# Performance work log

Measured on AMD Instinct MI355X. Metric: run time of the kernel, lower is better.

The kernel has to match this reference:

```python
import jax, jax.numpy as jnp
import numpy as np

N, E, IN, OUT, R, B = 20000, 640000, 128, 128, 65, 65
BN_EPS = 1e-5


def setup_inputs() -> dict:
    key = jax.random.key(0)
    ks = jax.random.split(key, 8)
    node_feats = jax.random.normal(ks[0], (N, IN), dtype=jnp.float32)
    src = jax.random.randint(ks[1], (E,), 0, N, dtype=jnp.int32)
    dst = jax.random.randint(ks[2], (E,), 0, N, dtype=jnp.int32)
    etype = jax.random.randint(ks[3], (E,), 0, R, dtype=jnp.int32)
    norm = jax.random.uniform(ks[4], (E, 1), dtype=jnp.float32)
    basis = jax.random.normal(ks[5], (B, IN, OUT), dtype=jnp.float32) * 0.05
    comp = jax.random.normal(ks[6], (R, B), dtype=jnp.float32) * 0.1
    h_bias = jnp.zeros((OUT,), dtype=jnp.float32)
    W_res = jax.random.normal(ks[7], (IN, OUT), dtype=jnp.float32) * 0.05
    b_res = jnp.zeros((OUT,), dtype=jnp.float32)
    gamma = jnp.ones((OUT,), dtype=jnp.float32)
    beta = jnp.zeros((OUT,), dtype=jnp.float32)
    return dict(node_feats=node_feats, src=src, dst=dst, etype=etype, norm=norm,
                basis=basis, comp=comp, h_bias=h_bias, W_res=W_res, b_res=b_res,
                gamma=gamma, beta=beta)


def reference(node_feats, src, dst, etype, norm, basis, comp, h_bias, W_res, b_res, gamma, beta):
    n, in_f = node_feats.shape
    r = comp.shape[0]
    # Basis decomposition: W_r = sum_b comp[r,b] * basis[b]  -> (R, in, out)
    W = jnp.einsum('rb,bio->rio', comp, basis)
    # Per-edge message x[src] * norm (norm is scalar per edge so it commutes
    # with the relation matmul). Aggregate per (dst, relation) first, then do
    # one dense relation-batched GEMM (mathematically identical to DGL's
    # per-edge transform + scatter-add, since everything is linear).
    msg = node_feats[src] * norm                       # (E, in)
    seg = dst.astype(jnp.int32) * r + etype            # combined (dst, rel) key
    S = jax.ops.segment_sum(msg, seg, num_segments=n * r).reshape(n, r, in_f)
    h = jnp.einsum('nri,rio->no', S, W) + h_bias       # (N, out)
    h = jax.nn.relu(h)                                 # conv activation (dropout p=0)
    # Residual branch: relu(Linear(x))
    h = h + jax.nn.relu(node_feats @ W_res + b_res)
    # BatchNorm1d (training mode: batch stats, biased variance)
    mean = jnp.mean(h, axis=0)
    var = jnp.var(h, axis=0)
    h = (h - mean) * jax.lax.rsqrt(var + BN_EPS) * gamma + beta
    return h
```

## Files before the change

### kernel.cpp

```cpp
#include <hip/hip_runtime.h>
#include <hip/hip_bf16.h>


#define N_NODES 20000
#define E_EDGES 640000
#define R_REL   65
#define TM      64
#define NB_RESID 313
#define MAX_TILES 10240
#define SCAT_CH 2560

typedef __attribute__((ext_vector_type(8))) short bf16x8;
typedef __attribute__((ext_vector_type(4))) float f32x4;
typedef __attribute__((ext_vector_type(4))) unsigned int u32x4;
typedef __attribute__((ext_vector_type(2))) unsigned int u32x2;

__device__ __forceinline__ unsigned short f2bf(float x) {
    union { float f; unsigned int u; } c; c.f = x;
    unsigned int b = c.u + 0x7fffu + ((c.u >> 16) & 1u);
    return (unsigned short)(b >> 16);
}
__device__ __forceinline__ float bf2f_lo(unsigned int u) {
    union { unsigned int u; float f; } c; c.u = u << 16; return c.f;
}
__device__ __forceinline__ float bf2f_hi(unsigned int u) {
    union { unsigned int u; float f; } c; c.u = u & 0xffff0000u; return c.f;
}
__device__ __forceinline__ void async16(const void* g, void* l) {
    __builtin_amdgcn_global_load_lds(
        (const __attribute__((address_space(1))) unsigned int*)g,
        (__attribute__((address_space(3))) unsigned int*)l, 16, 0, 0);
}
__device__ __forceinline__ int unperm(int p) {
    return (p & 64) + ((p & 3) << 4) + ((p >> 2) & 15);
}

__global__ void k_prep1(const float* __restrict__ comp, const float* __restrict__ basis,
                        float* __restrict__ W32, const int* __restrict__ et,
                        const int* __restrict__ dstA, int* __restrict__ ghist,
                        int* __restrict__ gh2, const float* __restrict__ node_feats,
                        unsigned short* __restrict__ node_bf) {
    __shared__ float lc[16 * 65];
    __shared__ int lh[R_REL];
    int b = blockIdx.x, t = threadIdx.x;
    if (b < 320) {
        int r0 = (b >> 6) * 16;
        int col = (b & 63) * 256 + t;
        for (int j = t; j < 16 * 65; j += 256) {
            int rr = r0 + j / 65;
            lc[j] = (rr < R_REL) ? comp[rr * 65 + (j % 65)] : 0.f;
        }
        __syncthreads();
        float acc[16];
#pragma unroll
        for (int j = 0; j < 16; ++j) acc[j] = 0.f;
        for (int k = 0; k < 65; ++k) {
            float v = basis[k * 16384 + col];
#pragma unroll
            for (int j = 0; j < 16; ++j) acc[j] += lc[j * 65 + k] * v;
        }
#pragma unroll
        for (int j = 0; j < 16; ++j) {
            int rr = r0 + j;
            if (rr < R_REL) W32[rr * 16384 + col] = acc[j];
        }
    } else if (b < 832) {
        if (t < R_REL) lh[t] = 0;
        __syncthreads();
        for (int i = (b - 320) * 256 + t; i < E_EDGES; i += 512 * 256) {
            atomicAdd(&lh[et[i]], 1);
            atomicAdd(&gh2[dstA[i]], 1);
        }
        __syncthreads();
        if (t < R_REL) atomicAdd(&ghist[t], lh[t]);
    } else {
        int i = (b - 832) * 256 + t;
        if (i < N_NODES * 32) {
            float4 v = reinterpret_cast<const float4*>(node_feats)[i];
            __hip_bfloat162 b0 = __float22bfloat162_rn(make_float2(v.x, v.y));
            __hip_bfloat162 b1 = __float22bfloat162_rn(make_float2(v.z, v.w));
            u32x2 pk;
            pk.x = *reinterpret_cast<unsigned int*>(&b0);
            pk.y = *reinterpret_cast<unsigned int*>(&b1);
            reinterpret_cast<u32x2*>(node_bf)[i] = pk;
        }
    }
}

__global__ void k_prep3(const int* __restrict__ gh2, int* __restrict__ cnt2,
                        int* __restrict__ seg, const int* __restrict__ ghist,
                        int* __restrict__ cnt, int* __restrict__ ntiles_p,
                        int* __restrict__ tile_rel, int* __restrict__ tile_start,
                        int* __restrict__ tile_len, const float* __restrict__ W32,
                        unsigned short* __restrict__ Wt, const float* __restrict__ Wresf,
                        unsigned short* __restrict__ Wrest) {
    int b = blockIdx.x, t = threadIdx.x;
    if (b < 80) {
        __shared__ int red[256];
        __shared__ int pref;
        int acc = 0;
        for (int i = t; i < b * 256; i += 256) acc += gh2[i];
        red[t] = acc;
        __syncthreads();
        for (int off = 128; off > 0; off >>= 1) {
            if (t < off) red[t] += red[t + off];
            __syncthreads();
        }
        if (t == 0) pref = red[0];
        __syncthreads();
        int i = b * 256 + t;
        int v = (i < N_NODES) ? gh2[i] : 0;
        red[t] = v;
        __syncthreads();
        for (int off = 1; off < 256; off <<= 1) {
            int x = (t >= off) ? red[t - off] : 0;
            __syncthreads();
            red[t] += x;
            __syncthreads();
        }
        int excl = red[t] - v + pref;
        if (i < N_NODES) {
            cnt2[i] = excl;
            seg[i] = excl;
            if (i == N_NODES - 1) seg[N_NODES] = excl + v;
        }
    } else if (b == 80) {
        __shared__ int base[R_REL + 1], tbase[R_REL + 1];
        int lane = t & 63;
        if (t < 64) {
            int v = ghist[lane];
            int x = v;
#pragma unroll
            for (int off = 1; off < 64; off <<= 1) {
                int y = __shfl_up(x, off);
                if (lane >= off) x += y;
            }
            base[lane] = x - v;
            if (lane == 63) {
                base[64] = x;
                base[65] = x + ghist[64];
            }
        }
        __syncthreads();
        if (t == 0) {
            int tb = 0;
            for (int r = 0; r < R_REL; ++r) {
                tbase[r] = tb;
                tb += (base[r + 1] - base[r] + TM - 1) / TM;
            }
            *ntiles_p = tb;
        }
        __syncthreads();
        if (t < R_REL) {
            cnt[t] = base[t];
            int s = base[t], e = base[t + 1], j = tbase[t];
            while (s < e) {
                int len = min(TM, e - s);
                tile_rel[j] = t; tile_start[j] = s; tile_len[j] = len;
                ++j; s += len;
            }
        }
    } else {
        __shared__ float tile[64][65];
        int bb = b - 81;
        const float* s; unsigned short* d; int sub;
        if (bb < R_REL * 4) { s = W32 + (size_t)(bb >> 2) * 16384; d = Wt + (size_t)(bb >> 2) * 16384; sub = bb & 3; }
        else { s = Wresf; d = Wrest; sub = bb - R_REL * 4; }
        int ot = (sub >> 1) & 1, itl = sub & 1;
        int tx = t & 63, ty = t >> 6;
        for (int it = 0; it < 16; ++it) {
            int i = ty + it * 4;
            tile[i][tx] = s[(itl * 64 + i) * 128 + ot * 64 + tx];
        }
        __syncthreads();
        for (int it = 0; it < 16; ++it) {
            int o = ty + it * 4;
            d[(ot * 64 + o) * 128 + itl * 64 + tx] = f2bf(tile[tx][o]);
        }
    }
}

__global__ void k_scatter2(const int* __restrict__ et, const int* __restrict__ srcA,
                           const int* __restrict__ dstA, const float* __restrict__ norm,
                           int* __restrict__ cnt, int* __restrict__ cnt2,
                           int* __restrict__ srcp, float* __restrict__ normp,
                           int* __restrict__ inv2) {
    __shared__ int lh[R_REL], lbase[R_REL];
    int c0 = blockIdx.x * SCAT_CH;
    int cend = min(c0 + SCAT_CH, E_EDGES);
    if (threadIdx.x < R_REL) lh[threadIdx.x] = 0;
    __syncthreads();
    for (int i = c0 + threadIdx.x; i < cend; i += 256) atomicAdd(&lh[et[i]], 1);
    __syncthreads();
    if (threadIdx.x < R_REL && lh[threadIdx.x] > 0)
        lbase[threadIdx.x] = atomicAdd(&cnt[threadIdx.x], lh[threadIdx.x]);
    __syncthreads();
    if (threadIdx.x < R_REL) lh[threadIdx.x] = 0;
    __syncthreads();
    for (int i = c0 + threadIdx.x; i < cend; i += 256) {
        int r = et[i];
        int p = lbase[r] + atomicAdd(&lh[r], 1);
        srcp[p] = srcA[i];
        normp[p] = norm[i];
        inv2[p] = atomicAdd(&cnt2[dstA[i]], 1);
    }
}

__global__ __launch_bounds__(256, 3) void k_conv_gemm(
    const int* __restrict__ tile_rel, const int* __restrict__ tile_start,
    const int* __restrict__ tile_len, const int* __restrict__ ntiles_p,
    const int* __restrict__ srcp, const float* __restrict__ normp,
    const unsigned short* __restrict__ node_bf,
    const unsigned short* __restrict__ Wt, const unsigned short* __restrict__ Wrest,
    const float* __restrict__ b_res, const int* __restrict__ inv2,
    unsigned short* __restrict__ t_out, float* __restrict__ resid) {
    __shared__ unsigned short Alds[64 * 128];
    __shared__ unsigned short Blds[128 * 128];
    __shared__ float snorm[64];
    __shared__ int sp2[64];
    int t = threadIdx.x;
    int w = t >> 6, lane = t & 63;
    int wr = (w >> 1) * 32, wc = (w & 1) * 64;
    int lrow = lane & 15, quad = lane >> 4;

    if (blockIdx.x < NB_RESID) {
        int row0 = blockIdx.x * 64;
        int nrows = min(64, N_NODES - row0);
#pragma unroll
        for (int it = 0; it < 8; ++it) {
            int j = t + 256 * it;
            int o = j >> 4, c = j & 15, cs = c ^ (o & 15);
            async16(Wrest + o * 128 + cs * 8, &Blds[o * 128 + c * 8]);
        }
#pragma unroll
        for (int it = 0; it < 4; ++it) {
            int j = t + 256 * it;
            int p = j >> 4, c = j & 15, cs = c ^ (p & 15);
            if (p < nrows)
                async16(node_bf + (size_t)(row0 + p) * 128 + cs * 8,
                        &Alds[p * 128 + c * 8]);
        }
        __syncthreads();
        f32x4 acc[2][4];
#pragma unroll
        for (int i = 0; i < 2; ++i)
#pragma unroll
            for (int j = 0; j < 4; ++j) acc[i][j] = (f32x4){0.f, 0.f, 0.f, 0.f};
#pragma unroll
        for (int ks = 0; ks < 4; ++ks) {
            int cs = (ks * 4 + quad) ^ lrow;
            bf16x8 af[2], bfr[4];
#pragma unroll
            for (int i = 0; i < 2; ++i)
                af[i] = *reinterpret_cast<const bf16x8*>(&Alds[(wr + i * 16 + lrow) * 128 + cs * 8]);
#pragma unroll
            for (int j = 0; j < 4; ++j)
                bfr[j] = *reinterpret_cast<const bf16x8*>(&Blds[(wc + j * 16 + lrow) * 128 + cs * 8]);
#pragma unroll
            for (int i = 0; i < 2; ++i)
#pragma unroll
                for (int j = 0; j < 4; ++j)
                    acc[i][j] = __builtin_amdgcn_mfma_f32_16x16x32_bf16(af[i], bfr[j], acc[i][j], 0, 0, 0);
        }
        float br0 = b_res[wc + lrow];
        float br1 = b_res[wc + 16 + lrow];
        float br2 = b_res[wc + 32 + lrow];
        float br3 = b_res[wc + 48 + lrow];
#pragma unroll
        for (int i = 0; i < 2; ++i) {
#pragma unroll
            for (int reg = 0; reg < 4; ++reg) {
                int grow = row0 + wr + i * 16 + quad * 4 + reg;
                if (grow < N_NODES) {
                    float4 v;
                    v.x = fmaxf(acc[i][0][reg] + br0, 0.f);
                    v.y = fmaxf(acc[i][1][reg] + br1, 0.f);
                    v.z = fmaxf(acc[i][2][reg] + br2, 0.f);
                    v.w = fmaxf(acc[i][3][reg] + br3, 0.f);
                    *reinterpret_cast<float4*>(resid + (size_t)grow * 128 + wc + lrow * 4) = v;
                }
            }
        }
        return;
    }

    int tid = blockIdx.x - NB_RESID;
    if (tid >= *ntiles_p) return;
    int r = tile_rel[tid], start = tile_start[tid], len = tile_len[tid];
    const unsigned short* Wr = Wt + (size_t)r * 16384;
#pragma unroll
    for (int it = 0; it < 8; ++it) {
        int j = t + 256 * it;
        int o = j >> 4, c = j & 15, cs = c ^ (o & 15);
        async16(Wr + o * 128 + cs * 8, &Blds[o * 128 + c * 8]);
    }
#pragma unroll
    for (int it = 0; it < 4; ++it) {
        int j = t + 256 * it;
        int p = j >> 4, c = j & 15, cs = c ^ (p & 15);
        if (p < len)
            async16(node_bf + (size_t)srcp[start + p] * 128 + cs * 8,
                    &Alds[p * 128 + c * 8]);
    }
    if (t < TM && t < len) {
        snorm[t] = normp[start + t];
        sp2[t] = inv2[start + t];
    }
    __syncthreads();

    f32x4 acc[2][4];
#pragma unroll
    for (int i = 0; i < 2; ++i)
#pragma unroll
        for (int j = 0; j < 4; ++j) acc[i][j] = (f32x4){0.f, 0.f, 0.f, 0.f};
#pragma unroll
    for (int ks = 0; ks < 4; ++ks) {
        int cs = (ks * 4 + quad) ^ lrow;
        bf16x8 af[2], bfr[4];
#pragma unroll
        for (int i = 0; i < 2; ++i)
            af[i] = *reinterpret_cast<const bf16x8*>(&Alds[(wr + i * 16 + lrow) * 128 + cs * 8]);
#pragma unroll
        for (int j = 0; j < 4; ++j)
            bfr[j] = *reinterpret_cast<const bf16x8*>(&Blds[(wc + j * 16 + lrow) * 128 + cs * 8]);
#pragma unroll
        for (int i = 0; i < 2; ++i)
#pragma unroll
            for (int j = 0; j < 4; ++j)
                acc[i][j] = __builtin_amdgcn_mfma_f32_16x16x32_bf16(af[i], bfr[j], acc[i][j], 0, 0, 0);
    }

#pragma unroll
    for (int i = 0; i < 2; ++i) {
        int m0 = wr + i * 16 + quad * 4;
#pragma unroll
        for (int reg = 0; reg < 4; ++reg) {
            int m = m0 + reg;
            if (m < len) {
                float nm = snorm[m];
                int p2 = sp2[m];
                float2 lo2 = make_float2(acc[i][0][reg] * nm, acc[i][1][reg] * nm);
                float2 hi2 = make_float2(acc[i][2][reg] * nm, acc[i][3][reg] * nm);
                __hip_bfloat162 blo = __float22bfloat162_rn(lo2);
                __hip_bfloat162 bhi = __float22bfloat162_rn(hi2);
                u32x2 st;
                st.x = *reinterpret_cast<unsigned int*>(&blo);
                st.y = *reinterpret_cast<unsigned int*>(&bhi);
                *reinterpret_cast<u32x2*>(t_out + (size_t)p2 * 128 + wc + lrow * 4) = st;
            }
        }
    }
}

__global__ __launch_bounds__(256) void k_reduce_fused(
    const unsigned short* __restrict__ t, const int* __restrict__ seg,
    const float* __restrict__ resid, const float* __restrict__ h_bias,
    float* __restrict__ h, float* __restrict__ colsum, float* __restrict__ colsumsq) {
    __shared__ float cs1[128], cs2[128], sbias[128];
    if (threadIdx.x < 128) {
        cs1[threadIdx.x] = 0.f; cs2[threadIdx.x] = 0.f;
        sbias[threadIdx.x] = h_bias[unperm(threadIdx.x)];
    }
    __syncthreads();
    int w = threadIdx.x >> 6, lane = threadIdx.x & 63;
    int g = lane >> 4, c = lane & 15;
    for (int k = 0; k < 4; ++k) {
        int d = blockIdx.x * 16 + k * 4 + w;
        int a = seg[d], b = seg[d + 1];
        float s[8];
#pragma unroll
        for (int kk = 0; kk < 8; ++kk) s[kk] = 0.f;
        int q = a + g;
        for (; q + 28 < b; q += 32) {
            u32x4 v0 = *reinterpret_cast<const u32x4*>(t + (size_t)q * 128 + c * 8);
            u32x4 v1 = *reinterpret_cast<const u32x4*>(t + (size_t)(q + 4) * 128 + c * 8);
            u32x4 v2 = *reinterpret_cast<const u32x4*>(t + (size_t)(q + 8) * 128 + c * 8);
            u32x4 v3 = *reinterpret_cast<const u32x4*>(t + (size_t)(q + 12) * 128 + c * 8);
            u32x4 v4 = *reinterpret_cast<const u32x4*>(t + (size_t)(q + 16) * 128 + c * 8);
            u32x4 v5 = *reinterpret_cast<const u32x4*>(t + (size_t)(q + 20) * 128 + c * 8);
            u32x4 v6 = *reinterpret_cast<const u32x4*>(t + (size_t)(q + 24) * 128 + c * 8);
            u32x4 v7 = *reinterpret_cast<const u32x4*>(t + (size_t)(q + 28) * 128 + c * 8);
#pragma unroll
            for (int kk = 0; kk < 4; ++kk) {
                s[2 * kk]     += bf2f_lo(v0[kk]) + bf2f_lo(v1[kk]) + bf2f_lo(v2[kk]) + bf2f_lo(v3[kk])
                               + bf2f_lo(v4[kk]) + bf2f_lo(v5[kk]) + bf2f_lo(v6[kk]) + bf2f_lo(v7[kk]);
                s[2 * kk + 1] += bf2f_hi(v0[kk]) + bf2f_hi(v1[kk]) + bf2f_hi(v2[kk]) + bf2f_hi(v3[kk])
                               + bf2f_hi(v4[kk]) + bf2f_hi(v5[kk]) + bf2f_hi(v6[kk]) + bf2f_hi(v7[kk]);
            }
        }
        for (; q < b; q += 4) {
            u32x4 v = *reinterpret_cast<const u32x4*>(t + (size_t)q * 128 + c * 8);
#pragma unroll
            for (int kk = 0; kk < 4; ++kk) {
                s[2 * kk]     += bf2f_lo(v[kk]);
                s[2 * kk + 1] += bf2f_hi(v[kk]);
            }
        }
#pragma unroll
        for (int kk = 0; kk < 8; ++kk) {
            s[kk] += __shfl_xor(s[kk], 16);
            s[kk] += __shfl_xor(s[kk], 32);
        }
        if (g == 0) {
            const float* rp = resid + (size_t)d * 128 + c * 8;
            float4 r0 = *reinterpret_cast<const float4*>(rp);
            float4 r1 = *reinterpret_cast<const float4*>(rp + 4);
            float rr[8] = {r0.x, r0.y, r0.z, r0.w, r1.x, r1.y, r1.z, r1.w};
            float v[8];
#pragma unroll
            for (int kk = 0; kk < 8; ++kk)
                v[kk] = fmaxf(s[kk] + sbias[c * 8 + kk], 0.f) + rr[kk];
            float* hp = h + (size_t)d * 128 + c * 8;
            *reinterpret_cast<float4*>(hp)     = make_float4(v[0], v[1], v[2], v[3]);
            *reinterpret_cast<float4*>(hp + 4) = make_float4(v[4], v[5], v[6], v[7]);
#pragma unroll
            for (int kk = 0; kk < 8; ++kk) {
                atomicAdd(&cs1[c * 8 + kk], v[kk]);
                atomicAdd(&cs2[c * 8 + kk], v[kk] * v[kk]);
            }
        }
    }
    __syncthreads();
    if (threadIdx.x < 128) {
        atomicAdd(&colsum[threadIdx.x], cs1[threadIdx.x]);
        atomicAdd(&colsumsq[threadIdx.x], cs2[threadIdx.x]);
    }
}

__global__ void k_bn(float* __restrict__ h, const float* __restrict__ colsum,
                     const float* __restrict__ colsumsq, const float* __restrict__ gamma,
                     const float* __restrict__ beta) {
    __shared__ float sc[128], sh[128], tile[8][128];
    int t = threadIdx.x;
    if (t < 128) {
        int n = unperm(t);
        float m = colsum[t] * (1.f / N_NODES);
        float var = colsumsq[t] * (1.f / N_NODES) - m * m;
        float s = gamma[n] * rsqrtf(var + 1e-5f);
        sc[t] = s;
        sh[t] = beta[n] - m * s;
    }
    __syncthreads();
    int r = t >> 5;
    int p0 = (t & 31) * 4;
    int n0 = (p0 & 64) + ((p0 >> 2) & 15);
    for (int row0 = blockIdx.x * 8; row0 < N_NODES; row0 += gridDim.x * 8) {
        int row = row0 + r;
        float4 v = make_float4(0.f, 0.f, 0.f, 0.f);
        if (row < N_NODES) v = *reinterpret_cast<float4*>(h + (size_t)row * 128 + p0);
        v.x = v.x * sc[p0] + sh[p0];
        v.y = v.y * sc[p0 + 1] + sh[p0 + 1];
        v.z = v.z * sc[p0 + 2] + sh[p0 + 2];
        v.w = v.w * sc[p0 + 3] + sh[p0 + 3];
        tile[r][n0]      = v.x;
        tile[r][n0 + 16] = v.y;
        tile[r][n0 + 32] = v.z;
        tile[r][n0 + 48] = v.w;
        __syncthreads();
        if (row < N_NODES)
            *reinterpret_cast<float4*>(h + (size_t)row * 128 + p0) =
                *reinterpret_cast<float4*>(&tile[r][p0]);
        __syncthreads();
    }
}

extern "C" void kernel_launch(void* const* d_in, const int* in_sizes, int n_in,
                              void* d_out, int out_size, void* d_ws, size_t ws_size,
                              hipStream_t stream) {
    (void)in_sizes; (void)n_in; (void)out_size; (void)ws_size;
    const float* node_feats = (const float*)d_in[0];
    const int* src    = (const int*)d_in[1];
    const int* dst    = (const int*)d_in[2];
    const int* etype  = (const int*)d_in[3];
    const float* norm = (const float*)d_in[4];
    const float* basis = (const float*)d_in[5];
    const float* comp  = (const float*)d_in[6];
    const float* h_bias = (const float*)d_in[7];
    const float* W_res  = (const float*)d_in[8];
    const float* b_res  = (const float*)d_in[9];
    const float* gamma  = (const float*)d_in[10];
    const float* beta   = (const float*)d_in[11];

    char* ws = (char*)d_ws;
    int* ghist      = (int*)(ws + 0);
    int* cnt        = (int*)(ws + 1024);
    int* ntiles_p   = (int*)(ws + 2048);
    float* colsum   = (float*)(ws + 2560);
    float* colsumsq = (float*)(ws + 3072);
    int* gh2        = (int*)(ws + 8192);
    int* tile_rel   = (int*)(ws + 88192);
    int* tile_start = (int*)(ws + 129152);
    int* tile_len   = (int*)(ws + 170112);
    unsigned short* Wt      = (unsigned short*)(ws + 211072);
    unsigned short* Wrest   = (unsigned short*)(ws + 2340992);
    unsigned short* node_bf = (unsigned short*)(ws + 2373760);
    int* srcp       = (int*)(ws + 7493760);
    float* normp    = (float*)(ws + 10053760);
    int* inv2       = (int*)(ws + 12613760);
    float* resid    = (float*)(ws + 15173760);
    int* seg        = (int*)(ws + 25413760);
    int* cnt2       = (int*)(ws + 25493776);
    const long T_BASE = 25573776L;
    float* W32      = (float*)(ws + T_BASE);
    unsigned short* t_buf = (unsigned short*)(ws + T_BASE);
    float* hacc = (float*)d_out;

    hipMemsetAsync(ws, 0, 88192, stream);
    k_prep1<<<3332, 256, 0, stream>>>(comp, basis, W32, etype, dst, ghist, gh2,
                                      node_feats, node_bf);
    k_prep3<<<345, 256, 0, stream>>>(gh2, cnt2, seg, ghist, cnt, ntiles_p,
                                     tile_rel, tile_start, tile_len,
                                     W32, Wt, W_res, Wrest);
    k_scatter2<<<(E_EDGES + SCAT_CH - 1) / SCAT_CH, 256, 0, stream>>>(
        etype, src, dst, norm, cnt, cnt2, srcp, normp, inv2);
    k_conv_gemm<<<NB_RESID + MAX_TILES, 256, 0, stream>>>(
        tile_rel, tile_start, tile_len, ntiles_p, srcp, normp, node_bf,
        Wt, Wrest, b_res, inv2, t_buf, resid);
    k_reduce_fused<<<N_NODES / 16, 256, 0, stream>>>(t_buf, seg, resid, h_bias,
                                                     hacc, colsum, colsumsq);
    k_bn<<<2500, 256, 0, stream>>>(hacc, colsum, colsumsq, gamma, beta);
}
```

Before: 325.1 us.

## Group edges by 64-node dst block and relation, accumulate in LDS

Edges are now bucketed by (dst>>6, relation) in place of relation-only tiles. Each block owns one 64-node destination group, half the relations and half the output columns. It runs the per-relation GEMMs and accumulates messages into a shared-memory tile, then writes partial sums. This drops the bf16 per-edge intermediate buffer and the separate segmented reduction, at the cost of reloading W per relation per group and running many small, unevenly filled tiles. A small combine kernel adds the two partials, the bias, ReLU and the residual, and the BN permutation is removed.

```diff
diff --git a/kernel.cpp b/kernel.cpp
--- a/kernel.cpp
+++ b/kernel.cpp
@@ -5,14 +5,13 @@
 #define N_NODES 20000
 #define E_EDGES 640000
 #define R_REL   65
-#define TM      64
-#define NB_RESID 313
-#define MAX_TILES 10240
-#define SCAT_CH 2560
+#define NGRP    313
+#define NKEY    (NGRP * R_REL)
+#define NB_CONV (NGRP * 4)
+#define NB_RES  (NGRP * 2)
 
 typedef __attribute__((ext_vector_type(8))) short bf16x8;
 typedef __attribute__((ext_vector_type(4))) float f32x4;
-typedef __attribute__((ext_vector_type(4))) unsigned int u32x4;
 typedef __attribute__((ext_vector_type(2))) unsigned int u32x2;
 
 __device__ __forceinline__ unsigned short f2bf(float x) {
@@ -20,28 +19,18 @@
     unsigned int b = c.u + 0x7fffu + ((c.u >> 16) & 1u);
     return (unsigned short)(b >> 16);
 }
-__device__ __forceinline__ float bf2f_lo(unsigned int u) {
-    union { unsigned int u; float f; } c; c.u = u << 16; return c.f;
-}
-__device__ __forceinline__ float bf2f_hi(unsigned int u) {
-    union { unsigned int u; float f; } c; c.u = u & 0xffff0000u; return c.f;
-}
 __device__ __forceinline__ void async16(const void* g, void* l) {
     __builtin_amdgcn_global_load_lds(
         (const __attribute__((address_space(1))) unsigned int*)g,
         (__attribute__((address_space(3))) unsigned int*)l, 16, 0, 0);
 }
-__device__ __forceinline__ int unperm(int p) {
-    return (p & 64) + ((p & 3) << 4) + ((p >> 2) & 15);
-}
 
 __global__ void k_prep1(const float* __restrict__ comp, const float* __restrict__ basis,
                         float* __restrict__ W32, const int* __restrict__ et,
-                        const int* __restrict__ dstA, int* __restrict__ ghist,
-                        int* __restrict__ gh2, const float* __restrict__ node_feats,
+                        const int* __restrict__ dstA, int* __restrict__ gh3,
+                        const float* __restrict__ node_feats,
                         unsigned short* __restrict__ node_bf) {
     __shared__ float lc[16 * 65];
-    __shared__ int lh[R_REL];
     int b = blockIdx.x, t = threadIdx.x;
     if (b < 320) {
         int r0 = (b >> 6) * 16;
@@ -65,14 +54,8 @@
             if (rr < R_REL) W32[rr * 16384 + col] = acc[j];
         }
     } else if (b < 832) {
-        if (t < R_REL) lh[t] = 0;
-        __syncthreads();
-        for (int i = (b - 320) * 256 + t; i < E_EDGES; i += 512 * 256) {
-            atomicAdd(&lh[et[i]], 1);
-            atomicAdd(&gh2[dstA[i]], 1);
-        }
-        __syncthreads();
-        if (t < R_REL) atomicAdd(&ghist[t], lh[t]);
+        for (int i = (b - 320) * 256 + t; i < E_EDGES; i += 512 * 256)
+            atomicAdd(&gh3[(dstA[i] >> 6) * 65 + et[i]], 1);
     } else {
         int i = (b - 832) * 256 + t;
         if (i < N_NODES * 32) {
@@ -87,11 +70,8 @@
     }
 }
 
-__global__ void k_prep3(const int* __restrict__ gh2, int* __restrict__ cnt2,
-                        int* __restrict__ seg, const int* __restrict__ ghist,
-                        int* __restrict__ cnt, int* __restrict__ ntiles_p,
-                        int* __restrict__ tile_rel, int* __restrict__ tile_start,
-                        int* __restrict__ tile_len, const float* __restrict__ W32,
+__global__ void k_prep2(const int* __restrict__ gh3, int* __restrict__ segK,
+                        int* __restrict__ cnt3, const float* __restrict__ W32,
                         unsigned short* __restrict__ Wt, const float* __restrict__ Wresf,
                         unsigned short* __restrict__ Wrest) {
     int b = blockIdx.x, t = threadIdx.x;
@@ -99,7 +79,7 @@
         __shared__ int red[256];
         __shared__ int pref;
         int acc = 0;
-        for (int i = t; i < b * 256; i += 256) acc += gh2[i];
+        for (int i = t; i < b * 256; i += 256) acc += gh3[i];
         red[t] = acc;
         __syncthreads();
         for (int off = 128; off > 0; off >>= 1) {
@@ -109,7 +89,7 @@
         if (t == 0) pref = red[0];
         __syncthreads();
         int i = b * 256 + t;
-        int v = (i < N_NODES) ? gh2[i] : 0;
+        int v = (i < NKEY) ? gh3[i] : 0;
         red[t] = v;
         __syncthreads();
         for (int off = 1; off < 256; off <<= 1) {
@@ -119,50 +99,14 @@
             __syncthreads();
         }
         int excl = red[t] - v + pref;
-        if (i < N_NODES) {
-            cnt2[i] = excl;
-            seg[i] = excl;
-            if (i == N_NODES - 1) seg[N_NODES] = excl + v;
-        }
-    } else if (b == 80) {
-        __shared__ int base[R_REL + 1], tbase[R_REL + 1];
-        int lane = t & 63;
-        if (t < 64) {
-            int v = ghist[lane];
-            int x = v;
-#pragma unroll
-            for (int off = 1; off < 64; off <<= 1) {
-                int y = __shfl_up(x, off);
-                if (lane >= off) x += y;
-            }
-            base[lane] = x - v;
-            if (lane == 63) {
-                base[64] = x;
-                base[65] = x + ghist[64];
-            }
-        }
-        __syncthreads();
-        if (t == 0) {
-            int tb = 0;
-            for (int r = 0; r < R_REL; ++r) {
-                tbase[r] = tb;
-                tb += (base[r + 1] - base[r] + TM - 1) / TM;
-            }
-            *ntiles_p = tb;
-        }
-        __syncthreads();
-        if (t < R_REL) {
-            cnt[t] = base[t];
-            int s = base[t], e = base[t + 1], j = tbase[t];
-            while (s < e) {
-                int len = min(TM, e - s);
-                tile_rel[j] = t; tile_start[j] = s; tile_len[j] = len;
-                ++j; s += len;
-            }
+        if (i < NKEY) {
+            segK[i] = excl;
+            cnt3[i] = excl;
+            if (i == NKEY - 1) segK[NKEY] = excl + v;
         }
     } else {
         __shared__ float tile[64][65];
-        int bb = b - 81;
+        int bb = b - 80;
         const float* s; unsigned short* d; int sub;
         if (bb < R_REL * 4) { s = W32 + (size_t)(bb >> 2) * 16384; d = Wt + (size_t)(bb >> 2) * 16384; sub = bb & 3; }
         else { s = Wresf; d = Wrest; sub = bb - R_REL * 4; }
@@ -180,287 +124,215 @@
     }
 }
 
-__global__ void k_scatter2(const int* __restrict__ et, const int* __restrict__ srcA,
-                           const int* __restrict__ dstA, const float* __restrict__ norm,
-                           int* __restrict__ cnt, int* __restrict__ cnt2,
-                           int* __restrict__ srcp, float* __restrict__ normp,
-                           int* __restrict__ inv2) {
-    __shared__ int lh[R_REL], lbase[R_REL];
-    int c0 = blockIdx.x * SCAT_CH;
-    int cend = min(c0 + SCAT_CH, E_EDGES);
-    if (threadIdx.x < R_REL) lh[threadIdx.x] = 0;
-    __syncthreads();
-    for (int i = c0 + threadIdx.x; i < cend; i += 256) atomicAdd(&lh[et[i]], 1);
-    __syncthreads();
-    if (threadIdx.x < R_REL && lh[threadIdx.x] > 0)
-        lbase[threadIdx.x] = atomicAdd(&cnt[threadIdx.x], lh[threadIdx.x]);
-    __syncthreads();
-    if (threadIdx.x < R_REL) lh[threadIdx.x] = 0;
-    __syncthreads();
-    for (int i = c0 + threadIdx.x; i < cend; i += 256) {
-        int r = et[i];
-        int p = lbase[r] + atomicAdd(&lh[r], 1);
-        srcp[p] = srcA[i];
-        normp[p] = norm[i];
-        inv2[p] = atomicAdd(&cnt2[dstA[i]], 1);
-    }
-}
-
-__global__ __launch_bounds__(256, 3) void k_conv_gemm(
-    const int* __restrict__ tile_rel, const int* __restrict__ tile_start,
-    const int* __restrict__ tile_len, const int* __restrict__ ntiles_p,
-    const int* __restrict__ srcp, const float* __restrict__ normp,
-    const unsigned short* __restrict__ node_bf,
+__global__ void k_scatter(const int* __restrict__ et, const int* __restrict__ srcA,
+                          const int* __restrict__ dstA, const float* __restrict__ norm,
+                          int* __restrict__ cnt3, int* __restrict__ ssd,
+                          float* __restrict__ normd) {
+    int i = blockIdx.x * 256 + threadIdx.x;
+    if (i >= E_EDGES) return;
+    int d = dstA[i];
+    int key = (d >> 6) * 65 + et[i];
+    int p = atomicAdd(&cnt3[key], 1);
+    ssd[p] = srcA[i] | ((d & 63) << 15);
+    normd[p] = norm[i];
+}
+
+__global__ __launch_bounds__(256, 3) void k_fused(
+    const int* __restrict__ segK, const int* __restrict__ ssd,
+    const float* __restrict__ normd, const unsigned short* __restrict__ node_bf,
     const unsigned short* __restrict__ Wt, const unsigned short* __restrict__ Wrest,
-    const float* __restrict__ b_res, const int* __restrict__ inv2,
-    unsigned short* __restrict__ t_out, float* __restrict__ resid) {
+    const float* __restrict__ b_res, float* __restrict__ hp0,
+    float* __restrict__ hp1, float* __restrict__ resid) {
     __shared__ unsigned short Alds[64 * 128];
-    __shared__ unsigned short Blds[128 * 128];
+    __shared__ unsigned short Blds[64 * 128];
+    __shared__ float hloc[64][65];
     __shared__ float snorm[64];
-    __shared__ int sp2[64];
+    __shared__ int sslot[64];
+    __shared__ int sseg[34];
     int t = threadIdx.x;
     int w = t >> 6, lane = t & 63;
-    int wr = (w >> 1) * 32, wc = (w & 1) * 64;
     int lrow = lane & 15, quad = lane >> 4;
-
-    if (blockIdx.x < NB_RESID) {
-        int row0 = blockIdx.x * 64;
+    int wc = (w >> 1) * 32;
+    int rbase = (w & 1) * 16;
+
+    if (blockIdx.x >= NB_CONV) {
+        int rb = blockIdx.x - NB_CONV;
+        int row0 = (rb >> 1) * 64, ch = rb & 1;
         int nrows = min(64, N_NODES - row0);
 #pragma unroll
-        for (int it = 0; it < 8; ++it) {
+        for (int it = 0; it < 4; ++it) {
             int j = t + 256 * it;
             int o = j >> 4, c = j & 15, cs = c ^ (o & 15);
-            async16(Wrest + o * 128 + cs * 8, &Blds[o * 128 + c * 8]);
+            async16(Wrest + (size_t)(ch * 64 + o) * 128 + cs * 8, &Blds[o * 128 + c * 8]);
         }
 #pragma unroll
         for (int it = 0; it < 4; ++it) {
             int j = t + 256 * it;
             int p = j >> 4, c = j & 15, cs = c ^ (p & 15);
             if (p < nrows)
-                async16(node_bf + (size_t)(row0 + p) * 128 + cs * 8,
-                        &Alds[p * 128 + c * 8]);
-        }
-        __syncthreads();
-        f32x4 acc[2][4];
-#pragma unroll
-        for (int i = 0; i < 2; ++i)
-#pragma unroll
-            for (int j = 0; j < 4; ++j) acc[i][j] = (f32x4){0.f, 0.f, 0.f, 0.f};
-#pragma unroll
-        for (int ks = 0; ks < 4; ++ks) {
-            int cs = (ks * 4 + quad) ^ lrow;
-            bf16x8 af[2], bfr[4];
-#pragma unroll
-            for (int i = 0; i < 2; ++i)
-                af[i] = *reinterpret_cast<const bf16x8*>(&Alds[(wr + i * 16 + lrow) * 128 + cs * 8]);
-#pragma unroll
-            for (int j = 0; j < 4; ++j)
-                bfr[j] = *reinterpret_cast<const bf16x8*>(&Blds[(wc + j * 16 + lrow) * 128 + cs * 8]);
-#pragma unroll
-            for (int i = 0; i < 2; ++i)
-#pragma unroll
-                for (int j = 0; j < 4; ++j)
-                    acc[i][j] = __builtin_amdgcn_mfma_f32_16x16x32_bf16(af[i], bfr[j], acc[i][j], 0, 0, 0);
-        }
-        float br0 = b_res[wc + lrow];
-        float br1 = b_res[wc + 16 + lrow];
-        float br2 = b_res[wc + 32 + lrow];
-        float br3 = b_res[wc + 48 + lrow];
-#pragma unroll
-        for (int i = 0; i < 2; ++i) {
+                async16(node_bf + (size_t)(row0 + p) * 128 + cs * 8, &Alds[p * 128 + c * 8]);
+        }
+        float bb0 = b_res[ch * 64 + wc + lrow];
+        float bb1 = b_res[ch * 64 + wc + 16 + lrow];
+        __syncthreads();
+#pragma unroll
+        for (int pass = 0; pass < 2; ++pass) {
+            int r0 = pass * 32 + rbase;
+            if (r0 >= nrows) break;
+            f32x4 acc0 = {0.f, 0.f, 0.f, 0.f}, acc1 = {0.f, 0.f, 0.f, 0.f};
+#pragma unroll
+            for (int ks = 0; ks < 4; ++ks) {
+                int cs = (ks * 4 + quad) ^ lrow;
+                bf16x8 a  = *reinterpret_cast<const bf16x8*>(&Alds[(r0 + lrow) * 128 + cs * 8]);
+                bf16x8 b0 = *reinterpret_cast<const bf16x8*>(&Blds[(wc + lrow) * 128 + cs * 8]);
+                bf16x8 b1 = *reinterpret_cast<const bf16x8*>(&Blds[(wc + 16 + lrow) * 128 + cs * 8]);
+                acc0 = __builtin_amdgcn_mfma_f32_16x16x32_bf16(a, b0, acc0, 0, 0, 0);
+                acc1 = __builtin_amdgcn_mfma_f32_16x16x32_bf16(a, b1, acc1, 0, 0, 0);
+            }
 #pragma unroll
             for (int reg = 0; reg < 4; ++reg) {
-                int grow = row0 + wr + i * 16 + quad * 4 + reg;
-                if (grow < N_NODES) {
-                    float4 v;
-                    v.x = fmaxf(acc[i][0][reg] + br0, 0.f);
-                    v.y = fmaxf(acc[i][1][reg] + br1, 0.f);
-                    v.z = fmaxf(acc[i][2][reg] + br2, 0.f);
-                    v.w = fmaxf(acc[i][3][reg] + br3, 0.f);
-                    *reinterpret_cast<float4*>(resid + (size_t)grow * 128 + wc + lrow * 4) = v;
+                int row = r0 + quad * 4 + reg;
+                if (row < nrows) {
+                    float* rp = resid + (size_t)(row0 + row) * 128 + ch * 64;
+                    rp[wc + lrow]      = fmaxf(acc0[reg] + bb0, 0.f);
+                    rp[wc + 16 + lrow] = fmaxf(acc1[reg] + bb1, 0.f);
                 }
             }
         }
         return;
     }
 
-    int tid = blockIdx.x - NB_RESID;
-    if (tid >= *ntiles_p) return;
-    int r = tile_rel[tid], start = tile_start[tid], len = tile_len[tid];
-    const unsigned short* Wr = Wt + (size_t)r * 16384;
-#pragma unroll
-    for (int it = 0; it < 8; ++it) {
-        int j = t + 256 * it;
-        int o = j >> 4, c = j & 15, cs = c ^ (o & 15);
-        async16(Wr + o * 128 + cs * 8, &Blds[o * 128 + c * 8]);
-    }
-#pragma unroll
-    for (int it = 0; it < 4; ++it) {
-        int j = t + 256 * it;
-        int p = j >> 4, c = j & 15, cs = c ^ (p & 15);
-        if (p < len)
-            async16(node_bf + (size_t)srcp[start + p] * 128 + cs * 8,
-                    &Alds[p * 128 + c * 8]);
-    }
-    if (t < TM && t < len) {
-        snorm[t] = normp[start + t];
-        sp2[t] = inv2[start + t];
-    }
-    __syncthreads();
-
-    f32x4 acc[2][4];
-#pragma unroll
-    for (int i = 0; i < 2; ++i)
-#pragma unroll
-        for (int j = 0; j < 4; ++j) acc[i][j] = (f32x4){0.f, 0.f, 0.f, 0.f};
-#pragma unroll
-    for (int ks = 0; ks < 4; ++ks) {
-        int cs = (ks * 4 + quad) ^ lrow;
-        bf16x8 af[2], bfr[4];
-#pragma unroll
-        for (int i = 0; i < 2; ++i)
-            af[i] = *reinterpret_cast<const bf16x8*>(&Alds[(wr + i * 16 + lrow) * 128 + cs * 8]);
-#pragma unroll
-        for (int j = 0; j < 4; ++j)
-            bfr[j] = *reinterpret_cast<const bf16x8*>(&Blds[(wc + j * 16 + lrow) * 128 + cs * 8]);
-#pragma unroll
-        for (int i = 0; i < 2; ++i)
-#pragma unroll
-            for (int j = 0; j < 4; ++j)
-                acc[i][j] = __builtin_amdgcn_mfma_f32_16x16x32_bf16(af[i], bfr[j], acc[i][j], 0, 0, 0);
-    }
-
-#pragma unroll
-    for (int i = 0; i < 2; ++i) {
-        int m0 = wr + i * 16 + quad * 4;
-#pragma unroll
-        for (int reg = 0; reg < 4; ++reg) {
-            int m = m0 + reg;
-            if (m < len) {
-                float nm = snorm[m];
-                int p2 = sp2[m];
-                float2 lo2 = make_float2(acc[i][0][reg] * nm, acc[i][1][reg] * nm);
-                float2 hi2 = make_float2(acc[i][2][reg] * nm, acc[i][3][reg] * nm);
-                __hip_bfloat162 blo = __float22bfloat162_rn(lo2);
-                __hip_bfloat162 bhi = __float22bfloat162_rn(hi2);
-                u32x2 st;
-                st.x = *reinterpret_cast<unsigned int*>(&blo);
-                st.y = *reinterpret_cast<unsigned int*>(&bhi);
-                *reinterpret_cast<u32x2*>(t_out + (size_t)p2 * 128 + wc + lrow * 4) = st;
-            }
-        }
-    }
-}
-
-__global__ __launch_bounds__(256) void k_reduce_fused(
-    const unsigned short* __restrict__ t, const int* __restrict__ seg,
+    int g = blockIdx.x >> 2;
+    int ch = (blockIdx.x >> 1) & 1, rh = blockIdx.x & 1;
+    int nrel = rh ? 32 : 33;
+    int key0 = g * 65 + rh * 33;
+    if (t <= nrel) sseg[t] = segK[key0 + t];
+    for (int i = t; i < 64 * 65; i += 256) (&hloc[0][0])[i] = 0.f;
+    __syncthreads();
+
+    for (int rr = 0; rr < nrel; ++rr) {
+        int base = sseg[rr], cnt = sseg[rr + 1] - base;
+        if (cnt == 0) continue;
+        int r = rh * 33 + rr;
+        for (int t0 = 0; t0 < cnt; t0 += 64) {
+            int rows = min(64, cnt - t0);
+            __syncthreads();
+            if (t0 == 0) {
+#pragma unroll
+                for (int it = 0; it < 4; ++it) {
+                    int j = t + 256 * it;
+                    int o = j >> 4, c = j & 15, cs = c ^ (o & 15);
+                    async16(Wt + (size_t)r * 16384 + (size_t)(ch * 64 + o) * 128 + cs * 8,
+                            &Blds[o * 128 + c * 8]);
+                }
+            }
+#pragma unroll
+            for (int it = 0; it < 4; ++it) {
+                int j = t + 256 * it;
+                int p = j >> 4, c = j & 15, cs = c ^ (p & 15);
+                if (p < rows) {
+                    int src = ssd[base + t0 + p] & 0x7fff;
+                    async16(node_bf + (size_t)src * 128 + cs * 8, &Alds[p * 128 + c * 8]);
+                }
+            }
+            if (t < rows) {
+                int pk = ssd[base + t0 + t];
+                sslot[t] = pk >> 15;
+                snorm[t] = normd[base + t0 + t];
+            }
+            __syncthreads();
+#pragma unroll
+            for (int pass = 0; pass < 2; ++pass) {
+                int r0 = pass * 32 + rbase;
+                if (r0 >= rows) break;
+                f32x4 acc0 = {0.f, 0.f, 0.f, 0.f}, acc1 = {0.f, 0.f, 0.f, 0.f};
+#pragma unroll
+                for (int ks = 0; ks < 4; ++ks) {
+                    int cs = (ks * 4 + quad) ^ lrow;
+                    bf16x8 a  = *reinterpret_cast<const bf16x8*>(&Alds[(r0 + lrow) * 128 + cs * 8]);
+                    bf16x8 b0 = *reinterpret_cast<const bf16x8*>(&Blds[(wc + lrow) * 128 + cs * 8]);
+                    bf16x8 b1 = *reinterpret_cast<const bf16x8*>(&Blds[(wc + 16 + lrow) * 128 + cs * 8]);
+                    acc0 = __builtin_amdgcn_mfma_f32_16x16x32_bf16(a, b0, acc0, 0, 0, 0);
+                    acc1 = __builtin_amdgcn_mfma_f32_16x16x32_bf16(a, b1, acc1, 0, 0, 0);
+                }
+#pragma unroll
+                for (int reg = 0; reg < 4; ++reg) {
+                    int row = r0 + quad * 4 + reg;
+                    if (row < rows) {
+                        float nm = snorm[row];
+                        int sl = sslot[row];
+                        atomicAdd(&hloc[sl][wc + lrow],      acc0[reg] * nm);
+                        atomicAdd(&hloc[sl][wc + 16 + lrow], acc1[reg] * nm);
+                    }
+                }
+            }
+        }
+    }
+    __syncthreads();
+    float* hp = rh ? hp1 : hp0;
+#pragma unroll
+    for (int it = 0; it < 16; ++it) {
+        int idx = t + 256 * it;
+        int sl = idx >> 6, c = idx & 63;
+        int node = g * 64 + sl;
+        if (node < N_NODES) hp[(size_t)node * 128 + ch * 64 + c] = hloc[sl][c];
+    }
+}
+
+__global__ __launch_bounds__(256) void k_combine(
+    const float* __restrict__ hp0, const float* __restrict__ hp1,
     const float* __restrict__ resid, const float* __restrict__ h_bias,
     float* __restrict__ h, float* __restrict__ colsum, float* __restrict__ colsumsq) {
     __shared__ float cs1[128], cs2[128], sbias[128];
-    if (threadIdx.x < 128) {
-        cs1[threadIdx.x] = 0.f; cs2[threadIdx.x] = 0.f;
-        sbias[threadIdx.x] = h_bias[unperm(threadIdx.x)];
-    }
-    __syncthreads();
-    int w = threadIdx.x >> 6, lane = threadIdx.x & 63;
-    int g = lane >> 4, c = lane & 15;
-    for (int k = 0; k < 4; ++k) {
-        int d = blockIdx.x * 16 + k * 4 + w;
-        int a = seg[d], b = seg[d + 1];
-        float s[8];
-#pragma unroll
-        for (int kk = 0; kk < 8; ++kk) s[kk] = 0.f;
-        int q = a + g;
-        for (; q + 28 < b; q += 32) {
-            u32x4 v0 = *reinterpret_cast<const u32x4*>(t + (size_t)q * 128 + c * 8);
-            u32x4 v1 = *reinterpret_cast<const u32x4*>(t + (size_t)(q + 4) * 128 + c * 8);
-            u32x4 v2 = *reinterpret_cast<const u32x4*>(t + (size_t)(q + 8) * 128 + c * 8);
-            u32x4 v3 = *reinterpret_cast<const u32x4*>(t + (size_t)(q + 12) * 128 + c * 8);
-            u32x4 v4 = *reinterpret_cast<const u32x4*>(t + (size_t)(q + 16) * 128 + c * 8);
-            u32x4 v5 = *reinterpret_cast<const u32x4*>(t + (size_t)(q + 20) * 128 + c * 8);
-            u32x4 v6 = *reinterpret_cast<const u32x4*>(t + (size_t)(q + 24) * 128 + c * 8);
-            u32x4 v7 = *reinterpret_cast<const u32x4*>(t + (size_t)(q + 28) * 128 + c * 8);
-#pragma unroll
-            for (int kk = 0; kk < 4; ++kk) {
-                s[2 * kk]     += bf2f_lo(v0[kk]) + bf2f_lo(v1[kk]) + bf2f_lo(v2[kk]) + bf2f_lo(v3[kk])
-                               + bf2f_lo(v4[kk]) + bf2f_lo(v5[kk]) + bf2f_lo(v6[kk]) + bf2f_lo(v7[kk]);
-                s[2 * kk + 1] += bf2f_hi(v0[kk]) + bf2f_hi(v1[kk]) + bf2f_hi(v2[kk]) + bf2f_hi(v3[kk])
-                               + bf2f_hi(v4[kk]) + bf2f_hi(v5[kk]) + bf2f_hi(v6[kk]) + bf2f_hi(v7[kk]);
-            }
-        }
-        for (; q < b; q += 4) {
-            u32x4 v = *reinterpret_cast<const u32x4*>(t + (size_t)q * 128 + c * 8);
-#pragma unroll
-            for (int kk = 0; kk < 4; ++kk) {
-                s[2 * kk]     += bf2f_lo(v[kk]);
-                s[2 * kk + 1] += bf2f_hi(v[kk]);
-            }
-        }
-#pragma unroll
-        for (int kk = 0; kk < 8; ++kk) {
-            s[kk] += __shfl_xor(s[kk], 16);
-            s[kk] += __shfl_xor(s[kk], 32);
-        }
-        if (g == 0) {
-            const float* rp = resid + (size_t)d * 128 + c * 8;
-            float4 r0 = *reinterpret_cast<const float4*>(rp);
-            float4 r1 = *reinterpret_cast<const float4*>(rp + 4);
-            float rr[8] = {r0.x, r0.y, r0.z, r0.w, r1.x, r1.y, r1.z, r1.w};
-            float v[8];
-#pragma unroll
-            for (int kk = 0; kk < 8; ++kk)
-                v[kk] = fmaxf(s[kk] + sbias[c * 8 + kk], 0.f) + rr[kk];
-            float* hp = h + (size_t)d * 128 + c * 8;
-            *reinterpret_cast<float4*>(hp)     = make_float4(v[0], v[1], v[2], v[3]);
-            *reinterpret_cast<float4*>(hp + 4) = make_float4(v[4], v[5], v[6], v[7]);
-#pragma unroll
-            for (int kk = 0; kk < 8; ++kk) {
-                atomicAdd(&cs1[c * 8 + kk], v[kk]);
-                atomicAdd(&cs2[c * 8 + kk], v[kk] * v[kk]);
-            }
-        }
-    }
-    __syncthreads();
-    if (threadIdx.x < 128) {
-        atomicAdd(&colsum[threadIdx.x], cs1[threadIdx.x]);
-        atomicAdd(&colsumsq[threadIdx.x], cs2[threadIdx.x]);
+    int t = threadIdx.x;
+    if (t < 128) { cs1[t] = 0.f; cs2[t] = 0.f; sbias[t] = h_bias[t]; }
+    __syncthreads();
+    int c4 = (t & 31) * 4;
+#pragma unroll
+    for (int pass = 0; pass < 2; ++pass) {
+        int row = blockIdx.x * 16 + pass * 8 + (t >> 5);
+        size_t off = (size_t)row * 128 + c4;
+        f32x4 va = *reinterpret_cast<const f32x4*>(hp0 + off);
+        f32x4 vb = *reinterpret_cast<const f32x4*>(hp1 + off);
+        f32x4 vr = *reinterpret_cast<const f32x4*>(resid + off);
+        f32x4 v;
+#pragma unroll
+        for (int k = 0; k < 4; ++k)
+            v[k] = fmaxf(va[k] + vb[k] + sbias[c4 + k], 0.f) + vr[k];
+        *reinterpret_cast<f32x4*>(h + off) = v;
+#pragma unroll
+        for (int k = 0; k < 4; ++k) {
+            atomicAdd(&cs1[c4 + k], v[k]);
+            atomicAdd(&cs2[c4 + k], v[k] * v[k]);
+        }
+    }
+    __syncthreads();
+    if (t < 128) {
+        atomicAdd(&colsum[t], cs1[t]);
+        atomicAdd(&colsumsq[t], cs2[t]);
     }
 }
 
 __global__ void k_bn(float* __restrict__ h, const float* __restrict__ colsum,
                      const float* __restrict__ colsumsq, const float* __restrict__ gamma,
                      const float* __restrict__ beta) {
-    __shared__ float sc[128], sh[128], tile[8][128];
+    __shared__ float sc[128], sh2[128];
     int t = threadIdx.x;
     if (t < 128) {
-        int n = unperm(t);
         float m = colsum[t] * (1.f / N_NODES);
         float var = colsumsq[t] * (1.f / N_NODES) - m * m;
-        float s = gamma[n] * rsqrtf(var + 1e-5f);
+        float s = gamma[t] * rsqrtf(var + 1e-5f);
         sc[t] = s;
-        sh[t] = beta[n] - m * s;
-    }
-    __syncthreads();
-    int r = t >> 5;
-    int p0 = (t & 31) * 4;
-    int n0 = (p0 & 64) + ((p0 >> 2) & 15);
-    for (int row0 = blockIdx.x * 8; row0 < N_NODES; row0 += gridDim.x * 8) {
-        int row = row0 + r;
-        float4 v = make_float4(0.f, 0.f, 0.f, 0.f);
-        if (row < N_NODES) v = *reinterpret_cast<float4*>(h + (size_t)row * 128 + p0);
-        v.x = v.x * sc[p0] + sh[p0];
-        v.y = v.y * sc[p0 + 1] + sh[p0 + 1];
-        v.z = v.z * sc[p0 + 2] + sh[p0 + 2];
-        v.w = v.w * sc[p0 + 3] + sh[p0 + 3];
-        tile[r][n0]      = v.x;
-        tile[r][n0 + 16] = v.y;
-        tile[r][n0 + 32] = v.z;
-        tile[r][n0 + 48] = v.w;
-        __syncthreads();
-        if (row < N_NODES)
-            *reinterpret_cast<float4*>(h + (size_t)row * 128 + p0) =
-                *reinterpret_cast<float4*>(&tile[r][p0]);
-        __syncthreads();
+        sh2[t] = beta[t] - m * s;
+    }
+    __syncthreads();
+    int i = blockIdx.x * 256 + t;
+    if (i < N_NODES * 32) {
+        int row = i >> 5, c4 = (i & 31) * 4;
+        f32x4 v = *reinterpret_cast<f32x4*>(h + (size_t)row * 128 + c4);
+#pragma unroll
+        for (int k = 0; k < 4; ++k) v[k] = v[k] * sc[c4 + k] + sh2[c4 + k];
+        *reinterpret_cast<f32x4*>(h + (size_t)row * 128 + c4) = v;
     }
 }
 
@@ -482,41 +354,29 @@
     const float* beta   = (const float*)d_in[11];
 
     char* ws = (char*)d_ws;
-    int* ghist      = (int*)(ws + 0);
-    int* cnt        = (int*)(ws + 1024);
-    int* ntiles_p   = (int*)(ws + 2048);
-    float* colsum   = (float*)(ws + 2560);
-    float* colsumsq = (float*)(ws + 3072);
-    int* gh2        = (int*)(ws + 8192);
-    int* tile_rel   = (int*)(ws + 88192);
-    int* tile_start = (int*)(ws + 129152);
-    int* tile_len   = (int*)(ws + 170112);
-    unsigned short* Wt      = (unsigned short*)(ws + 211072);
-    unsigned short* Wrest   = (unsigned short*)(ws + 2340992);
-    unsigned short* node_bf = (unsigned short*)(ws + 2373760);
-    int* srcp       = (int*)(ws + 7493760);
-    float* normp    = (float*)(ws + 10053760);
-    int* inv2       = (int*)(ws + 12613760);
-    float* resid    = (float*)(ws + 15173760);
-    int* seg        = (int*)(ws + 25413760);
-    int* cnt2       = (int*)(ws + 25493776);
-    const long T_BASE = 25573776L;
-    float* W32      = (float*)(ws + T_BASE);
-    unsigned short* t_buf = (unsigned short*)(ws + T_BASE);
-    float* hacc = (float*)d_out;
-
-    hipMemsetAsync(ws, 0, 88192, stream);
-    k_prep1<<<3332, 256, 0, stream>>>(comp, basis, W32, etype, dst, ghist, gh2,
+    float* colsum   = (float*)(ws + 0);
+    float* colsumsq = (float*)(ws + 512);
+    int* gh3        = (int*)(ws + 1024);
+    int* segK       = (int*)(ws + 82432);
+    int* cnt3       = (int*)(ws + 163840);
+    int* ssd        = (int*)(ws + 245248);
+    float* normd    = (float*)(ws + 2805248);
+    unsigned short* Wt      = (unsigned short*)(ws + 5365248);
+    unsigned short* Wrest   = (unsigned short*)(ws + 7495168);
+    unsigned short* node_bf = (unsigned short*)(ws + 7527936);
+    float* resid    = (float*)(ws + 12647936);
+    float* hp0      = (float*)(ws + 22887936);
+    float* hp1      = (float*)(ws + 33127936);
+    float* W32      = (float*)(ws + 43367936);
+    float* h = (float*)d_out;
+
+    hipMemsetAsync(ws, 0, 82432, stream);
+    k_prep1<<<3332, 256, 0, stream>>>(comp, basis, W32, etype, dst, gh3,
                                       node_feats, node_bf);
-    k_prep3<<<345, 256, 0, stream>>>(gh2, cnt2, seg, ghist, cnt, ntiles_p,
-                                     tile_rel, tile_start, tile_len,
-                                     W32, Wt, W_res, Wrest);
-    k_scatter2<<<(E_EDGES + SCAT_CH - 1) / SCAT_CH, 256, 0, stream>>>(
-        etype, src, dst, norm, cnt, cnt2, srcp, normp, inv2);
-    k_conv_gemm<<<NB_RESID + MAX_TILES, 256, 0, stream>>>(
-        tile_rel, tile_start, tile_len, ntiles_p, srcp, normp, node_bf,
-        Wt, Wrest, b_res, inv2, t_buf, resid);
-    k_reduce_fused<<<N_NODES / 16, 256, 0, stream>>>(t_buf, seg, resid, h_bias,
-                                                     hacc, colsum, colsumsq);
-    k_bn<<<2500, 256, 0, stream>>>(hacc, colsum, colsumsq, gamma, beta);
-}
+    k_prep2<<<344, 256, 0, stream>>>(gh3, segK, cnt3, W32, Wt, W_res, Wrest);
+    k_scatter<<<2500, 256, 0, stream>>>(etype, src, dst, norm, cnt3, ssd, normd);
+    k_fused<<<NB_CONV + NB_RES, 256, 0, stream>>>(segK, ssd, normd, node_bf,
+                                                  Wt, Wrest, b_res, hp0, hp1, resid);
+    k_combine<<<1250, 256, 0, stream>>>(hp0, hp1, resid, h_bias, h, colsum, colsumsq);
+    k_bn<<<2500, 256, 0, stream>>>(h, colsum, colsumsq, gamma, beta);
+}
```

Measured after the change: 749.6 us. +130.6%, slower.
